# Kernel optimization log

Hardware: AMD Instinct MI355X
Metric: run time of the kernel (lower is better)

Reference implementation:

```python
import jax, jax.numpy as jnp
import numpy as np

N, E = 50000, 800000
IN_C, HID, HEADS, OUT_C = 128, 64, 4, 64
NEG_SLOPE = 0.2


def _gat_layer(x, src, dst, W, a_src, a_dst, b, heads, out_dim, concat):
    n = x.shape[0]
    h = (x @ W).reshape(n, heads, out_dim)                      # [N,H,D]
    s_src = jnp.einsum('nhd,hd->nh', h, a_src)                  # [N,H]
    s_dst = jnp.einsum('nhd,hd->nh', h, a_dst)
    e = jax.nn.leaky_relu(s_src[src] + s_dst[dst], NEG_SLOPE)   # [Etot,H]
    m = jax.ops.segment_max(e, dst, num_segments=n)             # per-dst max (self-loops => no empty segments)
    w = jnp.exp(e - m[dst])
    denom = jax.ops.segment_sum(w, dst, num_segments=n)
    alpha = w / denom[dst]                                      # segment softmax over incoming edges
    msg = h[src] * alpha[..., None]                             # [Etot,H,D] edge gather + weight
    out = jax.ops.segment_sum(msg, dst, num_segments=n)         # scatter-sum aggregate
    out = out.reshape(n, heads * out_dim) if concat else out.mean(axis=1)
    return out + b


def setup_inputs() -> dict:
    key = jax.random.key(0)
    ks = jax.random.split(key, 10)
    x = jax.random.normal(ks[0], (N, IN_C), dtype=jnp.float32)
    edge_index = jax.random.randint(ks[1], (2, E), 0, N, dtype=jnp.int64)
    s1 = 1.0 / np.sqrt(IN_C)
    s2 = 1.0 / np.sqrt(HID * HEADS)
    return {
        'x': x,
        'edge_index': edge_index,
        'W1': jax.random.normal(ks[2], (IN_C, HEADS * HID), dtype=jnp.float32) * s1,
        'a_src1': jax.random.normal(ks[3], (HEADS, HID), dtype=jnp.float32) * s1,
        'a_dst1': jax.random.normal(ks[4], (HEADS, HID), dtype=jnp.float32) * s1,
        'b1': jnp.zeros((HEADS * HID,), dtype=jnp.float32),
        'W2': jax.random.normal(ks[5], (HEADS * HID, OUT_C), dtype=jnp.float32) * s2,
        'a_src2': jax.random.normal(ks[6], (1, OUT_C), dtype=jnp.float32) * s2,
        'a_dst2': jax.random.normal(ks[7], (1, OUT_C), dtype=jnp.float32) * s2,
        'b2': jnp.zeros((OUT_C,), dtype=jnp.float32),
    }


def reference(x, edge_index, W1, a_src1, a_dst1, b1, W2, a_src2, a_dst2, b2):
    n = x.shape[0]
    loop = jnp.arange(n, dtype=edge_index.dtype)
    src = jnp.concatenate([edge_index[0], loop])  # PyG GATConv adds self-loops
    dst = jnp.concatenate([edge_index[1], loop])
    # dropout layers are identity in eval mode
    h = _gat_layer(x, src, dst, W1, a_src1, a_dst1, b1, HEADS, HID, concat=True)
    h = jax.nn.elu(h)
    h = _gat_layer(h, src, dst, W2, a_src2, a_dst2, b2, 1, OUT_C, concat=False)
    return jnp.min(h, axis=0)
```

## Files before the change

kernel.cpp:

```cpp
#include <hip/hip_runtime.h>
#include <math.h>

typedef unsigned short ushort_t;
typedef __attribute__((ext_vector_type(8))) short bf16x8;
typedef __attribute__((ext_vector_type(4))) float f32x4;


__device__ inline unsigned fenc(float f) {
    unsigned u = __float_as_uint(f);
    return (u & 0x80000000u) ? ~u : (u | 0x80000000u);
}
__device__ inline float fdec(unsigned u) {
    return __uint_as_float((u & 0x80000000u) ? (u ^ 0x80000000u) : ~u);
}

__device__ inline float wrsum(float v) {
    #pragma unroll
    for (int m = 32; m; m >>= 1) v += __shfl_xor(v, m, 64);
    return v;
}
__device__ inline float lrelu(float x) { return x > 0.f ? x : 0.2f * x; }

__device__ inline ushort_t f2bf(float f) {
    unsigned u = __float_as_uint(f);
    u += 0x7FFFu + ((u >> 16) & 1u);
    return (ushort_t)(u >> 16);
}
__device__ inline float bflo(unsigned u) { return __uint_as_float(u << 16); }
__device__ inline float bfhi(unsigned u) { return __uint_as_float(u & 0xFFFF0000u); }

__global__ __launch_bounds__(256) void pre_kernel(const float* __restrict__ W1,
                                                  const float* __restrict__ W2,
                                                  const float* __restrict__ a_src2,
                                                  const float* __restrict__ a_dst2,
                                                  ushort_t* __restrict__ W1s,
                                                  ushort_t* __restrict__ W2s,
                                                  float* __restrict__ va,
                                                  float* __restrict__ vb,
                                                  int* __restrict__ deg,
                                                  unsigned* __restrict__ minenc,
                                                  int M) {
    int bid = blockIdx.x;
    int tid = threadIdx.x;
    if (bid < 128) {
        int idx = bid * 256 + tid;
        int j = idx & 7;
        int lane = (idx >> 3) & 63;
        int ct = (idx >> 9) & 15;
        int kc = (idx >> 13) & 3;
        int k = kc * 32 + (lane >> 4) * 8 + j;
        int c = ct * 16 + (lane & 15);
        W1s[idx] = f2bf(W1[k * 256 + c]);
    } else if (bid < 192) {
        int idx = (bid - 128) * 256 + tid;
        int j = idx & 7;
        int lane = (idx >> 3) & 63;
        int ct = (idx >> 9) & 3;
        int kc = idx >> 11;
        int k = kc * 32 + (lane >> 4) * 8 + j;
        int c = ct * 16 + (lane & 15);
        W2s[idx] = f2bf(W2[k * 64 + c]);
    } else if (bid == 192) {
        int k = tid;
        float sa = 0.f, sb = 0.f;
        #pragma unroll 8
        for (int c = 0; c < 64; c++) {
            float w = W2[k * 64 + c];
            sa += w * a_src2[c];
            sb += w * a_dst2[c];
        }
        va[k] = sa;
        vb[k] = sb;
        if (tid < 64) minenc[tid] = 0xFFFFFFFFu;
    } else {
        int t = (bid - 193) * 256 + tid;
        if (t < M) deg[t] = 0;
    }
}

__global__ __launch_bounds__(256) void front_kernel(const float* __restrict__ x,
                                                    const ushort_t* __restrict__ W1s,
                                                    const float* __restrict__ a_src,
                                                    const float* __restrict__ a_dst,
                                                    ushort_t* __restrict__ h1b,
                                                    float* __restrict__ ssrc,
                                                    float* __restrict__ sdst,
                                                    const int* __restrict__ ei,
                                                    int* __restrict__ deg,
                                                    int* __restrict__ rankb,
                                                    int N, int E, int Etot, int nb16) {
    __shared__ float ss[16 * 257];
    __shared__ float ps[256];
    int bid = blockIdx.x;
    int tid = threadIdx.x;

    if (bid >= nb16) {
        int i = (bid - nb16) * 256 + tid;
        if (i < Etot) {
            int d = (i < E) ? ei[E + i] : (i - E);
            rankb[i] = atomicAdd(&deg[d], 1);
        }
        return;
    }

    int base = bid * 16;
    {
        const float4* xv = (const float4*)(x + (size_t)base * 128);
        float4* xs4 = (float4*)ss;
        #pragma unroll
        for (int i = tid; i < 512; i += 256) {
            int row = i >> 5;
            float4 v = (base + row < N) ? xv[i] : make_float4(0.f, 0.f, 0.f, 0.f);
            xs4[row * 33 + (i & 31)] = v;
        }
    }
    __syncthreads();

    int lane = tid & 63, wv = tid >> 6;
    int m = lane & 15, q = lane >> 4;
    bf16x8 afrag[4];
    #pragma unroll
    for (int kc = 0; kc < 4; kc++) {
        const float* xp = ss + m * 132 + kc * 32 + q * 8;
        float4 xa = *(const float4*)xp;
        float4 xb = *(const float4*)(xp + 4);
        bf16x8 af;
        af[0] = (short)f2bf(xa.x); af[1] = (short)f2bf(xa.y);
        af[2] = (short)f2bf(xa.z); af[3] = (short)f2bf(xa.w);
        af[4] = (short)f2bf(xb.x); af[5] = (short)f2bf(xb.y);
        af[6] = (short)f2bf(xb.z); af[7] = (short)f2bf(xb.w);
        afrag[kc] = af;
    }
    __syncthreads();

    #pragma unroll
    for (int t = 0; t < 4; t++) {
        int ct = wv * 4 + t;
        f32x4 acc = {0.f, 0.f, 0.f, 0.f};
        #pragma unroll
        for (int kc = 0; kc < 4; kc++) {
            bf16x8 bfrag = *(const bf16x8*)(W1s + (((size_t)(kc * 16 + ct) * 64 + lane) << 3));
            acc = __builtin_amdgcn_mfma_f32_16x16x32_bf16(afrag[kc], bfrag, acc, 0, 0, 0);
        }
        #pragma unroll
        for (int reg = 0; reg < 4; reg++) {
            ss[(q * 4 + reg) * 257 + ct * 16 + m] = acc[reg];
        }
    }
    __syncthreads();

    int dd = tid & 63, jj = tid >> 6;
    #pragma unroll
    for (int t2 = 0; t2 < 4; t2++) {
        int j = jj + t2 * 4;
        int n = base + j;
        if (n < N) {
            const float* row = ss + j * 257;
            unsigned p0 = (unsigned)f2bf(row[dd]) | ((unsigned)f2bf(row[64 + dd]) << 16);
            unsigned p1 = (unsigned)f2bf(row[128 + dd]) | ((unsigned)f2bf(row[192 + dd]) << 16);
            *(uint2*)(h1b + (size_t)n * 256 + dd * 4) = make_uint2(p0, p1);
        }
    }
    int j = tid & 15, hh2 = (tid >> 4) & 3, which = (tid >> 6) & 1, half = tid >> 7;
    const float* av = which ? a_dst : a_src;
    int cbase = hh2 * 64 + half * 32;
    float sum = 0.f;
    #pragma unroll
    for (int i = 0; i < 32; i++) {
        int ii = (i + 8 * hh2) & 31;
        sum += ss[j * 257 + cbase + ii] * av[cbase + ii];
    }
    ps[tid] = sum;
    __syncthreads();
    if (half == 0) {
        float tot = sum + ps[tid + 128];
        int n = base + j;
        if (n < N) (which ? sdst : ssrc)[n * 4 + hh2] = tot;
    }
}

__global__ __launch_bounds__(256) void chunksum_kernel(const int* __restrict__ deg,
                                                       int* __restrict__ csum, int M) {
    __shared__ int sm[256];
    int t = blockIdx.x * 256 + threadIdx.x;
    sm[threadIdx.x] = (t < M) ? deg[t] : 0;
    __syncthreads();
    for (int off = 128; off > 0; off >>= 1) {
        if (threadIdx.x < off) sm[threadIdx.x] += sm[threadIdx.x + off];
        __syncthreads();
    }
    if (threadIdx.x == 0) csum[blockIdx.x] = sm[0];
}

__global__ __launch_bounds__(256) void scanchunks_kernel(const int* __restrict__ csum,
                                                         int* __restrict__ coffset, int nchunks) {
    __shared__ int sm[256];
    int v = (threadIdx.x < nchunks) ? csum[threadIdx.x] : 0;
    sm[threadIdx.x] = v;
    __syncthreads();
    for (int off = 1; off < 256; off <<= 1) {
        int a = (threadIdx.x >= off) ? sm[threadIdx.x - off] : 0;
        __syncthreads();
        sm[threadIdx.x] += a;
        __syncthreads();
    }
    coffset[threadIdx.x] = sm[threadIdx.x] - v;
}

__global__ __launch_bounds__(256) void rowptr_kernel(const int* __restrict__ deg,
                                                     const int* __restrict__ coffset,
                                                     int* __restrict__ rowptr, int M) {
    __shared__ int sm[256];
    int t = blockIdx.x * 256 + threadIdx.x;
    int v = (t < M) ? deg[t] : 0;
    sm[threadIdx.x] = v;
    __syncthreads();
    for (int off = 1; off < 256; off <<= 1) {
        int a = (threadIdx.x >= off) ? sm[threadIdx.x - off] : 0;
        __syncthreads();
        sm[threadIdx.x] += a;
        __syncthreads();
    }
    if (t < M) rowptr[t] = coffset[blockIdx.x] + sm[threadIdx.x] - v;
}

__global__ __launch_bounds__(256) void scatter_kernel(const int* __restrict__ ei,
                                                      const int* __restrict__ rowptr,
                                                      const int* __restrict__ rankb,
                                                      int* __restrict__ srcbuf, int E, int Etot) {
    int i = blockIdx.x * 256 + threadIdx.x;
    if (i >= Etot) return;
    int s, d;
    if (i < E) { s = ei[i]; d = ei[E + i]; } else { s = d = i - E; }
    srcbuf[rowptr[d] + rankb[i]] = s;
}

__global__ __launch_bounds__(256) void agg1_kernel(const int* __restrict__ rowptr,
                                                   const int* __restrict__ srcbuf,
                                                   const float* __restrict__ ssrc,
                                                   const float* __restrict__ sdst,
                                                   const ushort_t* __restrict__ h1b,
                                                   const float* __restrict__ b1,
                                                   const float* __restrict__ va,
                                                   const float* __restrict__ vb,
                                                   ushort_t* __restrict__ x2b,
                                                   float* __restrict__ ssrc2,
                                                   float* __restrict__ sdst2, int N) {
    __shared__ int    s_sh[4][64];
    __shared__ float4 w_sh[4][64];
    int lane = threadIdx.x & 63, w = threadIdx.x >> 6;
    int d = blockIdx.x * 4 + w;
    if (d >= N) return;
    int row = rowptr[d], end = rowptr[d + 1];
    float4 sd = *(const float4*)(sdst + d * 4);
    float l0 = 0.f, l1 = 0.f, l2 = 0.f, l3 = 0.f;
    float a0 = 0.f, a1 = 0.f, a2 = 0.f, a3 = 0.f;

    for (int base = row; base < end; base += 64) {
        int cnt = min(64, end - base);
        bool valid = lane < cnt;
        int s = valid ? srcbuf[base + lane] : 0;
        float4 ssv = *(const float4*)(ssrc + s * 4);
        float w0 = valid ? __expf(lrelu(ssv.x + sd.x)) : 0.f;
        float w1 = valid ? __expf(lrelu(ssv.y + sd.y)) : 0.f;
        float w2 = valid ? __expf(lrelu(ssv.z + sd.z)) : 0.f;
        float w3 = valid ? __expf(lrelu(ssv.w + sd.w)) : 0.f;
        l0 += wrsum(w0);  l1 += wrsum(w1);
        l2 += wrsum(w2);  l3 += wrsum(w3);
        s_sh[w][lane] = s;
        w_sh[w][lane] = make_float4(w0, w1, w2, w3);
        int cnt4 = (cnt + 3) & ~3;
        for (int j = 0; j < cnt4; j += 4) {
            int sj0 = s_sh[w][j], sj1 = s_sh[w][j + 1], sj2 = s_sh[w][j + 2], sj3 = s_sh[w][j + 3];
            float4 wj0 = w_sh[w][j], wj1 = w_sh[w][j + 1], wj2 = w_sh[w][j + 2], wj3 = w_sh[w][j + 3];
            uint2 u0 = *(const uint2*)(h1b + (size_t)sj0 * 256 + lane * 4);
            uint2 u1 = *(const uint2*)(h1b + (size_t)sj1 * 256 + lane * 4);
            uint2 u2 = *(const uint2*)(h1b + (size_t)sj2 * 256 + lane * 4);
            uint2 u3 = *(const uint2*)(h1b + (size_t)sj3 * 256 + lane * 4);
            a0 += wj0.x * bflo(u0.x); a1 += wj0.y * bfhi(u0.x);
            a2 += wj0.z * bflo(u0.y); a3 += wj0.w * bfhi(u0.y);
            a0 += wj1.x * bflo(u1.x); a1 += wj1.y * bfhi(u1.x);
            a2 += wj1.z * bflo(u1.y); a3 += wj1.w * bfhi(u1.y);
            a0 += wj2.x * bflo(u2.x); a1 += wj2.y * bfhi(u2.x);
            a2 += wj2.z * bflo(u2.y); a3 += wj2.w * bfhi(u2.y);
            a0 += wj3.x * bflo(u3.x); a1 += wj3.y * bfhi(u3.x);
            a2 += wj3.z * bflo(u3.y); a3 += wj3.w * bfhi(u3.y);
        }
    }
    float v0 = a0 / l0 + b1[lane];
    float v1 = a1 / l1 + b1[64 + lane];
    float v2 = a2 / l2 + b1[128 + lane];
    float v3 = a3 / l3 + b1[192 + lane];
    v0 = v0 > 0.f ? v0 : __expf(v0) - 1.f;
    v1 = v1 > 0.f ? v1 : __expf(v1) - 1.f;
    v2 = v2 > 0.f ? v2 : __expf(v2) - 1.f;
    v3 = v3 > 0.f ? v3 : __expf(v3) - 1.f;
    ushort_t* xp = x2b + (size_t)d * 256;
    xp[lane] = f2bf(v0); xp[64 + lane] = f2bf(v1);
    xp[128 + lane] = f2bf(v2); xp[192 + lane] = f2bf(v3);
    float sa = v0 * va[lane] + v1 * va[64 + lane] + v2 * va[128 + lane] + v3 * va[192 + lane];
    float sb = v0 * vb[lane] + v1 * vb[64 + lane] + v2 * vb[128 + lane] + v3 * vb[192 + lane];
    sa = wrsum(sa);
    sb = wrsum(sb);
    if (lane == 0) { ssrc2[d] = sa; sdst2[d] = sb; }
}

__global__ __launch_bounds__(256) void gemmz_kernel(const ushort_t* __restrict__ x2b,
                                                    const ushort_t* __restrict__ W2s,
                                                    const float* __restrict__ b2,
                                                    float* __restrict__ z, int N) {
    int base = blockIdx.x * 32;
    int tid = threadIdx.x;
    int lane = tid & 63, wv = tid >> 6;
    int m = lane & 15, q = lane >> 4;
    int c = wv * 16 + m;
    float bc = b2[c];

    #pragma unroll
    for (int h = 0; h < 2; h++) {
        int rbase = base + h * 16;
        bool rowok = (rbase + m) < N;
        const ushort_t* xrow = x2b + (size_t)(rbase + m) * 256;
        f32x4 acc = {0.f, 0.f, 0.f, 0.f};
        #pragma unroll
        for (int kc = 0; kc < 8; kc++) {
            bf16x8 af = {0, 0, 0, 0, 0, 0, 0, 0};
            if (rowok) af = *(const bf16x8*)(xrow + kc * 32 + q * 8);
            bf16x8 bf = *(const bf16x8*)(W2s + (((size_t)(kc * 4 + wv) * 64 + lane) << 3));
            acc = __builtin_amdgcn_mfma_f32_16x16x32_bf16(af, bf, acc, 0, 0, 0);
        }
        #pragma unroll
        for (int reg = 0; reg < 4; reg++) {
            int n = rbase + q * 4 + reg;
            if (n < N) z[(size_t)n * 64 + c] = acc[reg] + bc;
        }
    }
}

__global__ __launch_bounds__(256) void aggz_kernel(const int* __restrict__ rowptr,
                                                   const int* __restrict__ srcbuf,
                                                   const float* __restrict__ ssrc,
                                                   const float* __restrict__ sdst,
                                                   const float* __restrict__ z,
                                                   unsigned* __restrict__ minenc, int N) {
    __shared__ int   s_sh[4][64];
    __shared__ float w_sh[4][64];
    __shared__ float sm[256];
    int lane = threadIdx.x & 63, w = threadIdx.x >> 6;
    float minv = INFINITY;

    for (int d0 = blockIdx.x * 4; d0 < N; d0 += gridDim.x * 4) {
        int d = d0 + w;
        if (d < N) {
            int row = rowptr[d], end = rowptr[d + 1];
            float sdv = sdst[d];
            float l = 0.f;
            float a0 = 0.f, a1 = 0.f, a2 = 0.f, a3 = 0.f;
            for (int base = row; base < end; base += 64) {
                int cnt = min(64, end - base);
                bool valid = lane < cnt;
                int s = valid ? srcbuf[base + lane] : 0;
                float wt = valid ? __expf(lrelu(ssrc[s] + sdv)) : 0.f;
                l += wrsum(wt);
                s_sh[w][lane] = s;
                w_sh[w][lane] = wt;
                int cnt4 = (cnt + 3) & ~3;
                for (int j = 0; j < cnt4; j += 4) {
                    int sj0 = s_sh[w][j], sj1 = s_sh[w][j + 1];
                    int sj2 = s_sh[w][j + 2], sj3 = s_sh[w][j + 3];
                    float wj0 = w_sh[w][j], wj1 = w_sh[w][j + 1];
                    float wj2 = w_sh[w][j + 2], wj3 = w_sh[w][j + 3];
                    float z0 = z[(size_t)sj0 * 64 + lane];
                    float z1 = z[(size_t)sj1 * 64 + lane];
                    float z2 = z[(size_t)sj2 * 64 + lane];
                    float z3 = z[(size_t)sj3 * 64 + lane];
                    a0 += wj0 * z0; a1 += wj1 * z1;
                    a2 += wj2 * z2; a3 += wj3 * z3;
                }
            }
            float out = ((a0 + a1) + (a2 + a3)) / l;
            minv = fminf(minv, out);
        }
    }
    sm[threadIdx.x] = minv;
    __syncthreads();
    if (w == 0) {
        float v = fminf(fminf(sm[lane], sm[64 + lane]), fminf(sm[128 + lane], sm[192 + lane]));
        atomicMin(&minenc[lane], fenc(v));
    }
}

__global__ void decode_kernel(const unsigned* __restrict__ minenc, float* __restrict__ out) {
    int d = threadIdx.x;
    if (d < 64) out[d] = fdec(minenc[d]);
}

extern "C" void kernel_launch(void* const* d_in, const int* in_sizes, int n_in,
                              void* d_out, int out_size, void* d_ws, size_t ws_size,
                              hipStream_t stream) {
    const float* x      = (const float*)d_in[0];
    const int*   ei     = (const int*)d_in[1];
    const float* W1     = (const float*)d_in[2];
    const float* a_src1 = (const float*)d_in[3];
    const float* a_dst1 = (const float*)d_in[4];
    const float* b1     = (const float*)d_in[5];
    const float* W2     = (const float*)d_in[6];
    const float* a_src2 = (const float*)d_in[7];
    const float* a_dst2 = (const float*)d_in[8];
    const float* b2     = (const float*)d_in[9];
    float* out = (float*)d_out;

    const int N = in_sizes[0] / 128;
    const int E = in_sizes[1] / 2;
    const int Etot = E + N;
    const int Epad = Etot + 64;
    const int M = N + 1;
    const int nchunks = (M + 255) / 256;

    float* ws = (float*)d_ws;
    ushort_t* h1b = (ushort_t*)ws;
    ushort_t* x2b = (ushort_t*)(ws + (size_t)N * 128);
    float* z      = ws + (size_t)N * 256;
    ushort_t* W1s = (ushort_t*)(ws + (size_t)N * 320);
    ushort_t* W2s = (ushort_t*)(ws + (size_t)N * 320 + 16384);
    float* ssrc1  = ws + (size_t)N * 320 + 24576;
    float* sdst1  = ssrc1 + (size_t)N * 4;
    float* ssrc2  = sdst1 + (size_t)N * 4;
    float* sdst2  = ssrc2 + N;
    float* va     = sdst2 + N;
    float* vb     = va + 256;
    int*   deg    = (int*)(vb + 256);
    int*   rowptr = deg + M;
    int*   csum   = rowptr + M;
    int*   coff   = csum + 256;
    int*   srcbuf = coff + 256;
    int*   rankb  = srcbuf + Epad;
    unsigned* minenc = (unsigned*)(rankb + Epad);

    int nb16 = (N + 15) / 16;
    int nb32 = (N + 31) / 32;
    int nb4 = (N + 3) / 4;
    int nbh = (Etot + 255) / 256;
    int nbz = 1568;
    int nbdeg = (M + 255) / 256;

    pre_kernel<<<193 + nbdeg, 256, 0, stream>>>(W1, W2, a_src2, a_dst2, W1s, W2s,
                                                va, vb, deg, minenc, M);
    front_kernel<<<nb16 + nbh, 256, 0, stream>>>(x, W1s, a_src1, a_dst1, h1b, ssrc1, sdst1,
                                                 ei, deg, rankb, N, E, Etot, nb16);

    chunksum_kernel<<<nchunks, 256, 0, stream>>>(deg, csum, M);
    scanchunks_kernel<<<1, 256, 0, stream>>>(csum, coff, nchunks);
    rowptr_kernel<<<nchunks, 256, 0, stream>>>(deg, coff, rowptr, M);
    scatter_kernel<<<(Etot + 255) / 256, 256, 0, stream>>>(ei, rowptr, rankb, srcbuf, E, Etot);

    agg1_kernel<<<nb4, 256, 0, stream>>>(rowptr, srcbuf, ssrc1, sdst1, h1b, b1,
                                         va, vb, x2b, ssrc2, sdst2, N);
    gemmz_kernel<<<nb32, 256, 0, stream>>>(x2b, W2s, b2, z, N);
    aggz_kernel<<<nbz, 256, 0, stream>>>(rowptr, srcbuf, ssrc2, sdst2, z, minenc, N);
    decode_kernel<<<1, 64, 0, stream>>>(minenc, out);
}
```

Baseline: 297.3 us.

## Replace global-atomic CSR build with two-level bucketed counting sort

Destination-sorted CSR construction no longer counts degrees with global atomics and then does a three-kernel scan plus scatter. Edges are first bucketed by dst>>8 using LDS-atomic histograms per 4096-edge block, then scanned and scattered per bucket. Each bucket is then counting-sorted locally in LDS to produce rowptr and the final source list. This removes contended global atomics and random global scatters, at the cost of more kernel launches, extra passes over the edge arrays, and no longer overlapping edge counting with the front GEMM.

```diff
diff --git a/kernel.cpp b/kernel.cpp
--- a/kernel.cpp
+++ b/kernel.cpp
@@ -37,9 +37,7 @@
                                                   ushort_t* __restrict__ W2s,
                                                   float* __restrict__ va,
                                                   float* __restrict__ vb,
-                                                  int* __restrict__ deg,
-                                                  unsigned* __restrict__ minenc,
-                                                  int M) {
+                                                  unsigned* __restrict__ minenc) {
     int bid = blockIdx.x;
     int tid = threadIdx.x;
     if (bid < 128) {
@@ -60,7 +58,7 @@
         int k = kc * 32 + (lane >> 4) * 8 + j;
         int c = ct * 16 + (lane & 15);
         W2s[idx] = f2bf(W2[k * 64 + c]);
-    } else if (bid == 192) {
+    } else {
         int k = tid;
         float sa = 0.f, sb = 0.f;
         #pragma unroll 8
@@ -72,9 +70,126 @@
         va[k] = sa;
         vb[k] = sb;
         if (tid < 64) minenc[tid] = 0xFFFFFFFFu;
-    } else {
-        int t = (bid - 193) * 256 + tid;
-        if (t < M) deg[t] = 0;
+    }
+}
+
+__global__ __launch_bounds__(256) void hist_kernel(const int* __restrict__ ei,
+                                                   int* __restrict__ rnkbuf,
+                                                   int* __restrict__ bh,
+                                                   int E, int Etot, int NBA, int BB) {
+    __shared__ int h[256];
+    int t = threadIdx.x, blk = blockIdx.x;
+    h[t] = 0;
+    __syncthreads();
+    int i0 = blk * 4096 + t;
+    #pragma unroll
+    for (int e = 0; e < 16; e++) {
+        int i = i0 + e * 256;
+        if (i < Etot) {
+            int d = (i < E) ? ei[E + i] : (i - E);
+            int r = atomicAdd(&h[d >> 8], 1);
+            rnkbuf[i] = ((d >> 8) << 24) | ((d & 255) << 16) | r;
+        }
+    }
+    __syncthreads();
+    if (t < BB) bh[t * NBA + blk] = h[t];
+}
+
+__global__ __launch_bounds__(256) void scanb_kernel(int* __restrict__ bh,
+                                                    int* __restrict__ gtot, int NBA) {
+    __shared__ int sm[256];
+    int b = blockIdx.x, t = threadIdx.x;
+    int v = (t < NBA) ? bh[b * NBA + t] : 0;
+    sm[t] = v;
+    __syncthreads();
+    for (int o = 1; o < 256; o <<= 1) {
+        int a = (t >= o) ? sm[t - o] : 0;
+        __syncthreads();
+        sm[t] += a;
+        __syncthreads();
+    }
+    if (t < NBA) bh[b * NBA + t] = sm[t] - v;
+    if (t == 255) gtot[b] = sm[255];
+}
+
+__global__ __launch_bounds__(256) void scang_kernel(const int* __restrict__ gtot,
+                                                    int* __restrict__ bstart, int BB) {
+    __shared__ int sm[256];
+    int t = threadIdx.x;
+    int v = (t < BB) ? gtot[t] : 0;
+    sm[t] = v;
+    __syncthreads();
+    for (int o = 1; o < 256; o <<= 1) {
+        int a = (t >= o) ? sm[t - o] : 0;
+        __syncthreads();
+        sm[t] += a;
+        __syncthreads();
+    }
+    if (t < BB) bstart[t] = sm[t] - v;
+    if (t == BB - 1) bstart[BB] = sm[t];
+}
+
+__global__ __launch_bounds__(256) void scat_kernel(const int* __restrict__ ei,
+                                                   const int* __restrict__ rnkbuf,
+                                                   const int* __restrict__ bh,
+                                                   const int* __restrict__ bstart,
+                                                   int* __restrict__ srcbuf,
+                                                   int E, int Etot, int NBA, int BB) {
+    __shared__ int base[256];
+    int t = threadIdx.x, blk = blockIdx.x;
+    if (t < BB) base[t] = bstart[t] + bh[t * NBA + blk];
+    __syncthreads();
+    int i0 = blk * 4096 + t;
+    #pragma unroll
+    for (int e = 0; e < 16; e++) {
+        int i = i0 + e * 256;
+        if (i < Etot) {
+            unsigned u = (unsigned)rnkbuf[i];
+            int b = u >> 24;
+            int dl = (u >> 16) & 255;
+            int r = u & 0xFFFF;
+            int s = (i < E) ? ei[i] : (i - E);
+            srcbuf[base[b] + r] = s | (dl << 16);
+        }
+    }
+}
+
+__global__ __launch_bounds__(256) void csr_kernel(const int* __restrict__ bstart,
+                                                  int* __restrict__ srcbuf,
+                                                  int* __restrict__ rowptr, int N) {
+    __shared__ int eb[8192];
+    __shared__ unsigned short rr[8192];
+    __shared__ int h[256];
+    __shared__ int off[256];
+    int b = blockIdx.x, t = threadIdx.x;
+    int s0 = bstart[b];
+    int cnt = bstart[b + 1] - s0;
+    if (cnt > 8192) cnt = 8192;
+    h[t] = 0;
+    __syncthreads();
+    for (int j = t; j < cnt; j += 256) {
+        int u = srcbuf[s0 + j];
+        eb[j] = u;
+        rr[j] = (unsigned short)atomicAdd(&h[u >> 16], 1);
+    }
+    __syncthreads();
+    off[t] = h[t];
+    __syncthreads();
+    for (int o = 1; o < 256; o <<= 1) {
+        int a = (t >= o) ? off[t - o] : 0;
+        __syncthreads();
+        off[t] += a;
+        __syncthreads();
+    }
+    int excl = off[t] - h[t];
+    int d = b * 256 + t;
+    if (d <= N) rowptr[d] = s0 + excl;
+    __syncthreads();
+    h[t] = excl;
+    __syncthreads();
+    for (int j = t; j < cnt; j += 256) {
+        int u = eb[j];
+        srcbuf[s0 + h[u >> 16] + rr[j]] = u & 0xFFFF;
     }
 }
 
@@ -85,23 +200,11 @@
                                                     ushort_t* __restrict__ h1b,
                                                     float* __restrict__ ssrc,
                                                     float* __restrict__ sdst,
-                                                    const int* __restrict__ ei,
-                                                    int* __restrict__ deg,
-                                                    int* __restrict__ rankb,
-                                                    int N, int E, int Etot, int nb16) {
+                                                    int N) {
     __shared__ float ss[16 * 257];
     __shared__ float ps[256];
     int bid = blockIdx.x;
     int tid = threadIdx.x;
-
-    if (bid >= nb16) {
-        int i = (bid - nb16) * 256 + tid;
-        if (i < Etot) {
-            int d = (i < E) ? ei[E + i] : (i - E);
-            rankb[i] = atomicAdd(&deg[d], 1);
-        }
-        return;
-    }
 
     int base = bid * 16;
     {
@@ -177,62 +280,6 @@
         int n = base + j;
         if (n < N) (which ? sdst : ssrc)[n * 4 + hh2] = tot;
     }
-}
-
-__global__ __launch_bounds__(256) void chunksum_kernel(const int* __restrict__ deg,
-                                                       int* __restrict__ csum, int M) {
-    __shared__ int sm[256];
-    int t = blockIdx.x * 256 + threadIdx.x;
-    sm[threadIdx.x] = (t < M) ? deg[t] : 0;
-    __syncthreads();
-    for (int off = 128; off > 0; off >>= 1) {
-        if (threadIdx.x < off) sm[threadIdx.x] += sm[threadIdx.x + off];
-        __syncthreads();
-    }
-    if (threadIdx.x == 0) csum[blockIdx.x] = sm[0];
-}
-
-__global__ __launch_bounds__(256) void scanchunks_kernel(const int* __restrict__ csum,
-                                                         int* __restrict__ coffset, int nchunks) {
-    __shared__ int sm[256];
-    int v = (threadIdx.x < nchunks) ? csum[threadIdx.x] : 0;
-    sm[threadIdx.x] = v;
-    __syncthreads();
-    for (int off = 1; off < 256; off <<= 1) {
-        int a = (threadIdx.x >= off) ? sm[threadIdx.x - off] : 0;
-        __syncthreads();
-        sm[threadIdx.x] += a;
-        __syncthreads();
-    }
-    coffset[threadIdx.x] = sm[threadIdx.x] - v;
-}
-
-__global__ __launch_bounds__(256) void rowptr_kernel(const int* __restrict__ deg,
-                                                     const int* __restrict__ coffset,
-                                                     int* __restrict__ rowptr, int M) {
-    __shared__ int sm[256];
-    int t = blockIdx.x * 256 + threadIdx.x;
-    int v = (t < M) ? deg[t] : 0;
-    sm[threadIdx.x] = v;
-    __syncthreads();
-    for (int off = 1; off < 256; off <<= 1) {
-        int a = (threadIdx.x >= off) ? sm[threadIdx.x - off] : 0;
-        __syncthreads();
-        sm[threadIdx.x] += a;
-        __syncthreads();
-    }
-    if (t < M) rowptr[t] = coffset[blockIdx.x] + sm[threadIdx.x] - v;
-}
-
-__global__ __launch_bounds__(256) void scatter_kernel(const int* __restrict__ ei,
-                                                      const int* __restrict__ rowptr,
-                                                      const int* __restrict__ rankb,
-                                                      int* __restrict__ srcbuf, int E, int Etot) {
-    int i = blockIdx.x * 256 + threadIdx.x;
-    if (i >= Etot) return;
-    int s, d;
-    if (i < E) { s = ei[i]; d = ei[E + i]; } else { s = d = i - E; }
-    srcbuf[rowptr[d] + rankb[i]] = s;
 }
 
 __global__ __launch_bounds__(256) void agg1_kernel(const int* __restrict__ rowptr,
@@ -415,7 +462,9 @@
     const int Etot = E + N;
     const int Epad = Etot + 64;
     const int M = N + 1;
-    const int nchunks = (M + 255) / 256;
+
+    const int BB  = ((N - 1) >> 8) + 1;
+    const int NBA = (Etot + 4095) / 4096;
 
     float* ws = (float*)d_ws;
     ushort_t* h1b = (ushort_t*)ws;
@@ -429,30 +478,27 @@
     float* sdst2  = ssrc2 + N;
     float* va     = sdst2 + N;
     float* vb     = va + 256;
-    int*   deg    = (int*)(vb + 256);
-    int*   rowptr = deg + M;
-    int*   csum   = rowptr + M;
-    int*   coff   = csum + 256;
-    int*   srcbuf = coff + 256;
-    int*   rankb  = srcbuf + Epad;
-    unsigned* minenc = (unsigned*)(rankb + Epad);
+    int*   bh     = (int*)(vb + 256);
+    int*   rowptr = bh + M;
+    int*   gtot   = rowptr + M;
+    int*   bstart = gtot + 256;
+    int*   srcbuf = bstart + 256;
+    int*   rnkbuf = srcbuf + Epad;
+    unsigned* minenc = (unsigned*)(rnkbuf + Epad);
 
     int nb16 = (N + 15) / 16;
     int nb32 = (N + 31) / 32;
     int nb4 = (N + 3) / 4;
-    int nbh = (Etot + 255) / 256;
     int nbz = 1568;
-    int nbdeg = (M + 255) / 256;
-
-    pre_kernel<<<193 + nbdeg, 256, 0, stream>>>(W1, W2, a_src2, a_dst2, W1s, W2s,
-                                                va, vb, deg, minenc, M);
-    front_kernel<<<nb16 + nbh, 256, 0, stream>>>(x, W1s, a_src1, a_dst1, h1b, ssrc1, sdst1,
-                                                 ei, deg, rankb, N, E, Etot, nb16);
-
-    chunksum_kernel<<<nchunks, 256, 0, stream>>>(deg, csum, M);
-    scanchunks_kernel<<<1, 256, 0, stream>>>(csum, coff, nchunks);
-    rowptr_kernel<<<nchunks, 256, 0, stream>>>(deg, coff, rowptr, M);
-    scatter_kernel<<<(Etot + 255) / 256, 256, 0, stream>>>(ei, rowptr, rankb, srcbuf, E, Etot);
+
+    pre_kernel<<<193, 256, 0, stream>>>(W1, W2, a_src2, a_dst2, W1s, W2s, va, vb, minenc);
+    front_kernel<<<nb16, 256, 0, stream>>>(x, W1s, a_src1, a_dst1, h1b, ssrc1, sdst1, N);
+
+    hist_kernel<<<NBA, 256, 0, stream>>>(ei, rnkbuf, bh, E, Etot, NBA, BB);
+    scanb_kernel<<<BB, 256, 0, stream>>>(bh, gtot, NBA);
+    scang_kernel<<<1, 256, 0, stream>>>(gtot, bstart, BB);
+    scat_kernel<<<NBA, 256, 0, stream>>>(ei, rnkbuf, bh, bstart, srcbuf, E, Etot, NBA, BB);
+    csr_kernel<<<BB, 256, 0, stream>>>(bstart, srcbuf, rowptr, N);
 
     agg1_kernel<<<nb4, 256, 0, stream>>>(rowptr, srcbuf, ssrc1, sdst1, h1b, b1,
                                          va, vb, x2b, ssrc2, sdst2, N);
```

New measurement: 275.0 us. 7.5% less time.
